# Performance work log

Measured on AMD Instinct MI355X. Metric: run time of the kernel, lower is better.

Reference implementation:

```python
import jax, jax.numpy as jnp
import numpy as np

B, T, C, H = 1024, 256, 384, 64  # batch, block_size, n_embd, head_size


def _rope_tables():
    # standard rotary tables: theta_i = 10000^(-2i/H), angles = pos * theta
    inv_freq = 1.0 / (10000.0 ** (jnp.arange(0, H, 2, dtype=jnp.float32) / H))  # [H/2]
    pos = jnp.arange(T, dtype=jnp.float32)
    ang = pos[:, None] * inv_freq[None, :]          # [T, H/2]
    ang = jnp.concatenate([ang, ang], axis=-1)       # [T, H]
    return jnp.cos(ang), jnp.sin(ang)


def setup_inputs() -> dict:
    key = jax.random.key(0)
    kx, kq, kk, kv = jax.random.split(key, 4)
    cos, sin = _rope_tables()
    s = 1.0 / np.sqrt(C)
    return {
        "x": jax.random.normal(kx, (B, T, C), dtype=jnp.float32),
        "cos": cos,
        "sin": sin,
        "Wq": jax.random.normal(kq, (C, H), dtype=jnp.float32) * s,
        "Wk": jax.random.normal(kk, (C, H), dtype=jnp.float32) * s,
        "Wv": jax.random.normal(kv, (C, H), dtype=jnp.float32) * s,
    }


def _rotary(x, cos, sin):
    # x: [B, T, H]; cos/sin: [T, H]
    half = x.shape[-1] // 2
    x1, x2 = x[..., :half], x[..., half:]
    rotated = jnp.concatenate([-x2, x1], axis=-1)
    return x * cos + rotated * sin


def reference(x, cos, sin, Wq, Wk, Wv):
    Tn = x.shape[1]
    q = x @ Wq                                  # [B,T,H]
    k = x @ Wk
    v = x @ Wv
    q = _rotary(q, cos[:Tn], sin[:Tn])
    k = _rotary(k, cos[:Tn], sin[:Tn])
    scale = k.shape[-1] ** -0.5
    wei = jnp.einsum('btd,bsd->bts', q, k) * scale  # [B,T,T] — materialized as in original
    causal = jnp.tril(jnp.ones((Tn, Tn), dtype=bool))
    wei = jnp.where(causal, wei, -jnp.inf)
    wei = jax.nn.softmax(wei, axis=-1)
    # dropout omitted (eval mode / deterministic reference)
    out = jnp.einsum('bts,bsd->btd', wei, v)    # [B,T,H]
    return out
```

## Files before the change

### kernel.cpp

```cpp
#include <hip/hip_runtime.h>
#include <hip/hip_bf16.h>

typedef __attribute__((ext_vector_type(8))) short bf16x8;
typedef __attribute__((ext_vector_type(4))) float f32x4;

#define B_ 1024
#define T_ 256
#define C_ 384
#define H_ 64

__device__ __forceinline__ unsigned short f2bf(float f) {
  unsigned int u = __float_as_uint(f);
  return (unsigned short)((u + 0x7fffu + ((u >> 16) & 1u)) >> 16);
}

__global__ void pack_w(const float* __restrict__ Wq, const float* __restrict__ Wk,
                       const float* __restrict__ Wv, unsigned short* __restrict__ wt) {
  int id = blockIdx.x * 256 + threadIdx.x;
  if (id >= 192 * 384) return;
  int n = id / 384, k = id % 384;
  const float* W = (n < 64) ? Wq : ((n < 128) ? Wk : Wv);
  wt[id] = f2bf(W[k * 64 + (n & 63)]);
}

__launch_bounds__(512, 2)
__global__ void head_fused(const float* __restrict__ x, const float* __restrict__ cosp,
                           const float* __restrict__ sinp,
                           const unsigned short* __restrict__ wt,
                           float* __restrict__ out) {
  __shared__ unsigned short Klds[256 * 72];
  __shared__ unsigned short Vlds[64 * 264];
  __shared__ unsigned short Plds[8 * 16 * 264];

  const int tid = threadIdx.x;
  const int w = tid >> 6;
  const int lane = tid & 63;
  const int l15 = lane & 15;
  const int lq = lane >> 4;
  const int b = blockIdx.x;

  const float* xb = x + (size_t)b * T_ * C_;
  const int rt[2] = {w, 15 - w};

  f32x4 acc[2][12];
  #pragma unroll
  for (int i = 0; i < 2; ++i)
    #pragma unroll
    for (int nt = 0; nt < 12; ++nt) {
      f32x4 z = {0.f, 0.f, 0.f, 0.f};
      acc[i][nt] = z;
    }

  float4 px[2][2][2];
  #pragma unroll
  for (int s = 0; s < 2; ++s)
    #pragma unroll
    for (int i = 0; i < 2; ++i) {
      const float* p = xb + (rt[i] * 16 + l15) * C_ + s * 32 + lq * 8;
      px[s][i][0] = *(const float4*)p;
      px[s][i][1] = *(const float4*)(p + 4);
    }

  #pragma unroll
  for (int ks = 0; ks < 12; ++ks) {
    const int cur = ks & 1;
    const int k0 = ks * 32 + lq * 8;

    bf16x8 af[2];
    #pragma unroll
    for (int i = 0; i < 2; ++i) {
      bf16x8 a;
      a[0] = (short)f2bf(px[cur][i][0].x); a[1] = (short)f2bf(px[cur][i][0].y);
      a[2] = (short)f2bf(px[cur][i][0].z); a[3] = (short)f2bf(px[cur][i][0].w);
      a[4] = (short)f2bf(px[cur][i][1].x); a[5] = (short)f2bf(px[cur][i][1].y);
      a[6] = (short)f2bf(px[cur][i][1].z); a[7] = (short)f2bf(px[cur][i][1].w);
      af[i] = a;
    }

    bf16x8 bfv[12];
    #pragma unroll
    for (int nt = 0; nt < 12; ++nt)
      bfv[nt] = *(const bf16x8*)(wt + (nt * 16 + l15) * C_ + k0);

    if (ks + 2 < 12) {
      #pragma unroll
      for (int i = 0; i < 2; ++i) {
        const float* p = xb + (rt[i] * 16 + l15) * C_ + (ks + 2) * 32 + lq * 8;
        px[cur][i][0] = *(const float4*)p;
        px[cur][i][1] = *(const float4*)(p + 4);
      }
    }

    #pragma unroll
    for (int nt = 0; nt < 12; ++nt)
      #pragma unroll
      for (int i = 0; i < 2; ++i)
        acc[i][nt] = __builtin_amdgcn_mfma_f32_16x16x32_bf16(af[i], bfv[nt], acc[i][nt], 0, 0, 0);
  }

  #pragma unroll
  for (int i = 0; i < 2; ++i) {
    #pragma unroll
    for (int j = 0; j < 4; ++j) {
      int t = rt[i] * 16 + lq * 4 + j;
      #pragma unroll
      for (int h = 0; h < 2; ++h) {
        int c = h * 16 + l15;
        float cv = cosp[t * H_ + c];
        float sv = sinp[t * H_ + c];
        float a = acc[i][h][j], bb = acc[i][h + 2][j];
        acc[i][h][j]     = a * cv - bb * sv;
        acc[i][h + 2][j] = bb * cv + a * sv;
        float a2 = acc[i][4 + h][j], b2 = acc[i][6 + h][j];
        acc[i][4 + h][j] = a2 * cv - b2 * sv;
        acc[i][6 + h][j] = b2 * cv + a2 * sv;
      }
    }
  }

  unsigned short* Pw = Plds + w * 16 * 264;
  #pragma unroll
  for (int i = 0; i < 2; ++i) {
    #pragma unroll
    for (int j = 0; j < 4; ++j) {
      int t = rt[i] * 16 + lq * 4 + j;
      int qr = i * 16 + lq * 4 + j;
      #pragma unroll
      for (int nt = 0; nt < 4; ++nt) {
        Pw[qr * 72 + nt * 16 + l15]    = f2bf(acc[i][nt][j]);
        Klds[t * 72 + nt * 16 + l15]   = f2bf(acc[i][4 + nt][j]);
        Vlds[(nt * 16 + l15) * 264 + t] = f2bf(acc[i][8 + nt][j]);
      }
    }
  }

  bf16x8 aq[2][2];
  #pragma unroll
  for (int i = 0; i < 2; ++i)
    #pragma unroll
    for (int ks2 = 0; ks2 < 2; ++ks2)
      aq[i][ks2] = *(const bf16x8*)&Pw[(i * 16 + l15) * 72 + ks2 * 32 + lq * 8];

  __syncthreads();

  float* ob = out + (size_t)b * T_ * H_;

  #pragma unroll
  for (int i = 0; i < 2; ++i) {
    const int ti = rt[i];
    const int t0 = ti * 16;

    f32x4 sacc[16];
    #pragma unroll
    for (int si = 0; si < 16; ++si) {
      f32x4 z = {0.f, 0.f, 0.f, 0.f};
      sacc[si] = z;
    }

    #pragma unroll
    for (int si = 0; si < 16; ++si) {
      if (si <= ti) {
        #pragma unroll
        for (int ks2 = 0; ks2 < 2; ++ks2) {
          bf16x8 bk = *(const bf16x8*)&Klds[(si * 16 + l15) * 72 + ks2 * 32 + lq * 8];
          sacc[si] = __builtin_amdgcn_mfma_f32_16x16x32_bf16(aq[i][ks2], bk, sacc[si], 0, 0, 0);
        }
      }
    }

    int trow = t0 + lq * 4;
    #pragma unroll
    for (int si = 0; si < 16; ++si) {
      #pragma unroll
      for (int j = 0; j < 4; ++j) {
        float s = sacc[si][j] * 0.125f;
        if (si * 16 + l15 > trow + j) s = -1e30f;
        sacc[si][j] = s;
      }
    }

    float rl[4];
    #pragma unroll
    for (int j = 0; j < 4; ++j) {
      float mj = -1e30f;
      #pragma unroll
      for (int si = 0; si < 16; ++si) mj = fmaxf(mj, sacc[si][j]);
      #pragma unroll
      for (int d = 1; d < 16; d <<= 1) mj = fmaxf(mj, __shfl_xor(mj, d));
      float lj = 0.0f;
      #pragma unroll
      for (int si = 0; si < 16; ++si) {
        float p = __expf(sacc[si][j] - mj);
        lj += p;
        Pw[(lq * 4 + j) * 264 + si * 16 + l15] = f2bf(p);
      }
      #pragma unroll
      for (int d = 1; d < 16; d <<= 1) lj += __shfl_xor(lj, d);
      rl[j] = 1.0f / lj;
    }

    f32x4 oacc[4];
    #pragma unroll
    for (int nt = 0; nt < 4; ++nt) {
      f32x4 z = {0.f, 0.f, 0.f, 0.f};
      oacc[nt] = z;
    }
    int nk = (t0 + 16 + 31) >> 5;
    for (int ks2 = 0; ks2 < nk; ++ks2) {
      bf16x8 ap = *(const bf16x8*)&Pw[l15 * 264 + ks2 * 32 + lq * 8];
      #pragma unroll
      for (int nt = 0; nt < 4; ++nt) {
        bf16x8 bv = *(const bf16x8*)&Vlds[(nt * 16 + l15) * 264 + ks2 * 32 + lq * 8];
        oacc[nt] = __builtin_amdgcn_mfma_f32_16x16x32_bf16(ap, bv, oacc[nt], 0, 0, 0);
      }
    }

    #pragma unroll
    for (int nt = 0; nt < 4; ++nt)
      #pragma unroll
      for (int j = 0; j < 4; ++j)
        ob[(t0 + lq * 4 + j) * H_ + nt * 16 + l15] = oacc[nt][j] * rl[j];
  }
}

extern "C" void kernel_launch(void* const* d_in, const int* in_sizes, int n_in,
                              void* d_out, int out_size, void* d_ws, size_t ws_size,
                              hipStream_t stream) {
  const float* x    = (const float*)d_in[0];
  const float* cosp = (const float*)d_in[1];
  const float* sinp = (const float*)d_in[2];
  const float* Wq   = (const float*)d_in[3];
  const float* Wk   = (const float*)d_in[4];
  const float* Wv   = (const float*)d_in[5];
  unsigned short* wt = (unsigned short*)d_ws;
  float* out = (float*)d_out;

  pack_w<<<288, 256, 0, stream>>>(Wq, Wk, Wv, wt);
  head_fused<<<B_, 512, 0, stream>>>(x, cosp, sinp, wt, out);
}
```

Baseline: 241.3 us.

## Split fused head kernel into QKV projection and attention kernels via MFMA-fragment workspace

Splits the single fused per-batch kernel into a QKV projection kernel and an attention kernel. Each uses 256-thread blocks with two blocks per batch element, and they exchange Q/K/V through global workspace stored in MFMA-fragment-packed bf16 layout. Weights are also pre-packed into fragment order so each lane does a single contiguous vector load, and attention reads K/V fragments straight from global/L2 instead of LDS. The goal is more parallelism and occupancy with less LDS use, at the cost of an extra global round trip for Q/K/V (about 100MB) and an extra launch. The old fused path is kept as a fallback when the workspace is too small.

New measurement: 379.4 us. 1.57x slower.

```diff
diff --git a/kernel.cpp b/kernel.cpp
--- a/kernel.cpp
+++ b/kernel.cpp
@@ -14,33 +14,35 @@
   return (unsigned short)((u + 0x7fffu + ((u >> 16) & 1u)) >> 16);
 }
 
-__global__ void pack_w(const float* __restrict__ Wq, const float* __restrict__ Wk,
-                       const float* __restrict__ Wv, unsigned short* __restrict__ wt) {
+__global__ void pack_w_frag(const float* __restrict__ Wq, const float* __restrict__ Wk,
+                            const float* __restrict__ Wv, unsigned short* __restrict__ wtp) {
   int id = blockIdx.x * 256 + threadIdx.x;
-  if (id >= 192 * 384) return;
-  int n = id / 384, k = id % 384;
+  if (id >= 144 * 512) return;
+  int i = id & 7, lane = (id >> 3) & 63, f = id >> 9;
+  int nt = f % 12, ks = f / 12;
+  int n = nt * 16 + (lane & 15);
+  int k = ks * 32 + (lane >> 4) * 8 + i;
   const float* W = (n < 64) ? Wq : ((n < 128) ? Wk : Wv);
-  wt[id] = f2bf(W[k * 64 + (n & 63)]);
-}
-
-__launch_bounds__(512, 2)
-__global__ void head_fused(const float* __restrict__ x, const float* __restrict__ cosp,
+  wtp[id] = f2bf(W[k * 64 + (n & 63)]);
+}
+
+__launch_bounds__(256, 4)
+__global__ void qkv_kernel(const float* __restrict__ x, const float* __restrict__ cosp,
                            const float* __restrict__ sinp,
-                           const unsigned short* __restrict__ wt,
-                           float* __restrict__ out) {
-  __shared__ unsigned short Klds[256 * 72];
-  __shared__ unsigned short Vlds[64 * 264];
-  __shared__ unsigned short Plds[8 * 16 * 264];
-
+                           const unsigned short* __restrict__ wtp,
+                           unsigned short* __restrict__ qp,
+                           unsigned short* __restrict__ kp,
+                           unsigned short* __restrict__ vp) {
   const int tid = threadIdx.x;
   const int w = tid >> 6;
   const int lane = tid & 63;
   const int l15 = lane & 15;
   const int lq = lane >> 4;
-  const int b = blockIdx.x;
+  const int bk = blockIdx.x;
+  const int b = bk >> 1, half = bk & 1;
+  const int rt[2] = {half * 8 + w, half * 8 + 7 - w};
 
   const float* xb = x + (size_t)b * T_ * C_;
-  const int rt[2] = {w, 15 - w};
 
   f32x4 acc[2][12];
   #pragma unroll
@@ -64,8 +66,6 @@
   #pragma unroll
   for (int ks = 0; ks < 12; ++ks) {
     const int cur = ks & 1;
-    const int k0 = ks * 32 + lq * 8;
-
     bf16x8 af[2];
     #pragma unroll
     for (int i = 0; i < 2; ++i) {
@@ -76,12 +76,10 @@
       a[6] = (short)f2bf(px[cur][i][1].z); a[7] = (short)f2bf(px[cur][i][1].w);
       af[i] = a;
     }
-
     bf16x8 bfv[12];
     #pragma unroll
     for (int nt = 0; nt < 12; ++nt)
-      bfv[nt] = *(const bf16x8*)(wt + (nt * 16 + l15) * C_ + k0);
-
+      bfv[nt] = *(const bf16x8*)(wtp + ((ks * 12 + nt) * 64 + lane) * 8);
     if (ks + 2 < 12) {
       #pragma unroll
       for (int i = 0; i < 2; ++i) {
@@ -90,7 +88,6 @@
         px[cur][i][1] = *(const float4*)(p + 4);
       }
     }
-
     #pragma unroll
     for (int nt = 0; nt < 12; ++nt)
       #pragma unroll
@@ -118,6 +115,228 @@
     }
   }
 
+  #pragma unroll
+  for (int i = 0; i < 2; ++i) {
+    const int tile = rt[i];
+    #pragma unroll
+    for (int j = 0; j < 4; ++j) {
+      const int r = lq * 4 + j;
+      #pragma unroll
+      for (int nt = 0; nt < 4; ++nt) {
+        size_t qa = ((((size_t)b * 16 + tile) * 2 + (nt >> 1)) * 64 +
+                     ((nt & 1) * 2 + (l15 >> 3)) * 16 + r) * 8 + (l15 & 7);
+        qp[qa] = f2bf(acc[i][nt][j]);
+        kp[qa] = f2bf(acc[i][4 + nt][j]);
+        size_t va = ((((size_t)b * 4 + nt) * 8 + (tile >> 1)) * 64 +
+                     ((tile & 1) * 2 + (r >> 3)) * 16 + l15) * 8 + (r & 7);
+        vp[va] = f2bf(acc[i][8 + nt][j]);
+      }
+    }
+  }
+}
+
+__launch_bounds__(256, 4)
+__global__ void attn_kernel(const unsigned short* __restrict__ qp,
+                            const unsigned short* __restrict__ kp,
+                            const unsigned short* __restrict__ vp,
+                            float* __restrict__ out) {
+  __shared__ unsigned short Plds[4 * 16 * 264];
+
+  const int tid = threadIdx.x;
+  const int w = tid >> 6;
+  const int lane = tid & 63;
+  const int l15 = lane & 15;
+  const int lq = lane >> 4;
+  const int bk = blockIdx.x;
+  const int b = bk >> 1, half = bk & 1;
+  const int rt2[2] = {half * 8 + w, half * 8 + 7 - w};
+
+  unsigned short* Pw = Plds + w * 16 * 264;
+  float* ob = out + (size_t)b * T_ * H_;
+
+  #pragma unroll
+  for (int i = 0; i < 2; ++i) {
+    const int ti = rt2[i];
+    const int t0 = ti * 16;
+
+    bf16x8 aq[2];
+    #pragma unroll
+    for (int ks2 = 0; ks2 < 2; ++ks2)
+      aq[ks2] = *(const bf16x8*)(qp + ((((size_t)b * 16 + ti) * 2 + ks2) * 64 + lane) * 8);
+
+    f32x4 sacc[16];
+    #pragma unroll
+    for (int si = 0; si < 16; ++si) {
+      f32x4 z = {0.f, 0.f, 0.f, 0.f};
+      sacc[si] = z;
+    }
+
+    #pragma unroll
+    for (int si = 0; si < 16; ++si) {
+      if (si <= ti) {
+        #pragma unroll
+        for (int ks2 = 0; ks2 < 2; ++ks2) {
+          bf16x8 bkf = *(const bf16x8*)(kp + ((((size_t)b * 16 + si) * 2 + ks2) * 64 + lane) * 8);
+          sacc[si] = __builtin_amdgcn_mfma_f32_16x16x32_bf16(aq[ks2], bkf, sacc[si], 0, 0, 0);
+        }
+      }
+    }
+
+    int trow = t0 + lq * 4;
+    #pragma unroll
+    for (int si = 0; si < 16; ++si) {
+      #pragma unroll
+      for (int j = 0; j < 4; ++j) {
+        float s = sacc[si][j] * 0.125f;
+        if (si * 16 + l15 > trow + j) s = -1e30f;
+        sacc[si][j] = s;
+      }
+    }
+
+    float rl[4];
+    #pragma unroll
+    for (int j = 0; j < 4; ++j) {
+      float mj = -1e30f;
+      #pragma unroll
+      for (int si = 0; si < 16; ++si) mj = fmaxf(mj, sacc[si][j]);
+      #pragma unroll
+      for (int d = 1; d < 16; d <<= 1) mj = fmaxf(mj, __shfl_xor(mj, d));
+      float lj = 0.0f;
+      #pragma unroll
+      for (int si = 0; si < 16; ++si) {
+        float p = __expf(sacc[si][j] - mj);
+        lj += p;
+        Pw[(lq * 4 + j) * 264 + si * 16 + l15] = f2bf(p);
+      }
+      #pragma unroll
+      for (int d = 1; d < 16; d <<= 1) lj += __shfl_xor(lj, d);
+      rl[j] = 1.0f / lj;
+    }
+
+    f32x4 oacc[4];
+    #pragma unroll
+    for (int nt = 0; nt < 4; ++nt) {
+      f32x4 z = {0.f, 0.f, 0.f, 0.f};
+      oacc[nt] = z;
+    }
+    int nk = (t0 + 16 + 31) >> 5;
+    for (int ks = 0; ks < nk; ++ks) {
+      bf16x8 ap = *(const bf16x8*)&Pw[l15 * 264 + ks * 32 + lq * 8];
+      #pragma unroll
+      for (int nt = 0; nt < 4; ++nt) {
+        bf16x8 bv = *(const bf16x8*)(vp + ((((size_t)b * 4 + nt) * 8 + ks) * 64 + lane) * 8);
+        oacc[nt] = __builtin_amdgcn_mfma_f32_16x16x32_bf16(ap, bv, oacc[nt], 0, 0, 0);
+      }
+    }
+
+    #pragma unroll
+    for (int nt = 0; nt < 4; ++nt)
+      #pragma unroll
+      for (int j = 0; j < 4; ++j)
+        ob[(t0 + lq * 4 + j) * H_ + nt * 16 + l15] = oacc[nt][j] * rl[j];
+  }
+}
+
+__global__ void pack_w_rm(const float* __restrict__ Wq, const float* __restrict__ Wk,
+                          const float* __restrict__ Wv, unsigned short* __restrict__ wt) {
+  int id = blockIdx.x * 256 + threadIdx.x;
+  if (id >= 192 * 384) return;
+  int n = id / 384, k = id % 384;
+  const float* W = (n < 64) ? Wq : ((n < 128) ? Wk : Wv);
+  wt[id] = f2bf(W[k * 64 + (n & 63)]);
+}
+
+__launch_bounds__(512, 2)
+__global__ void head_fused(const float* __restrict__ x, const float* __restrict__ cosp,
+                           const float* __restrict__ sinp,
+                           const unsigned short* __restrict__ wt,
+                           float* __restrict__ out) {
+  __shared__ unsigned short Klds[256 * 72];
+  __shared__ unsigned short Vlds[64 * 264];
+  __shared__ unsigned short Plds[8 * 16 * 264];
+
+  const int tid = threadIdx.x;
+  const int w = tid >> 6;
+  const int lane = tid & 63;
+  const int l15 = lane & 15;
+  const int lq = lane >> 4;
+  const int b = blockIdx.x;
+
+  const float* xb = x + (size_t)b * T_ * C_;
+  const int rt[2] = {w, 15 - w};
+
+  f32x4 acc[2][12];
+  #pragma unroll
+  for (int i = 0; i < 2; ++i)
+    #pragma unroll
+    for (int nt = 0; nt < 12; ++nt) {
+      f32x4 z = {0.f, 0.f, 0.f, 0.f};
+      acc[i][nt] = z;
+    }
+
+  float4 px[2][2][2];
+  #pragma unroll
+  for (int s = 0; s < 2; ++s)
+    #pragma unroll
+    for (int i = 0; i < 2; ++i) {
+      const float* p = xb + (rt[i] * 16 + l15) * C_ + s * 32 + lq * 8;
+      px[s][i][0] = *(const float4*)p;
+      px[s][i][1] = *(const float4*)(p + 4);
+    }
+
+  #pragma unroll
+  for (int ks = 0; ks < 12; ++ks) {
+    const int cur = ks & 1;
+    const int k0 = ks * 32 + lq * 8;
+    bf16x8 af[2];
+    #pragma unroll
+    for (int i = 0; i < 2; ++i) {
+      bf16x8 a;
+      a[0] = (short)f2bf(px[cur][i][0].x); a[1] = (short)f2bf(px[cur][i][0].y);
+      a[2] = (short)f2bf(px[cur][i][0].z); a[3] = (short)f2bf(px[cur][i][0].w);
+      a[4] = (short)f2bf(px[cur][i][1].x); a[5] = (short)f2bf(px[cur][i][1].y);
+      a[6] = (short)f2bf(px[cur][i][1].z); a[7] = (short)f2bf(px[cur][i][1].w);
+      af[i] = a;
+    }
+    bf16x8 bfv[12];
+    #pragma unroll
+    for (int nt = 0; nt < 12; ++nt)
+      bfv[nt] = *(const bf16x8*)(wt + (nt * 16 + l15) * C_ + k0);
+    if (ks + 2 < 12) {
+      #pragma unroll
+      for (int i = 0; i < 2; ++i) {
+        const float* p = xb + (rt[i] * 16 + l15) * C_ + (ks + 2) * 32 + lq * 8;
+        px[cur][i][0] = *(const float4*)p;
+        px[cur][i][1] = *(const float4*)(p + 4);
+      }
+    }
+    #pragma unroll
+    for (int nt = 0; nt < 12; ++nt)
+      #pragma unroll
+      for (int i = 0; i < 2; ++i)
+        acc[i][nt] = __builtin_amdgcn_mfma_f32_16x16x32_bf16(af[i], bfv[nt], acc[i][nt], 0, 0, 0);
+  }
+
+  #pragma unroll
+  for (int i = 0; i < 2; ++i) {
+    #pragma unroll
+    for (int j = 0; j < 4; ++j) {
+      int t = rt[i] * 16 + lq * 4 + j;
+      #pragma unroll
+      for (int h = 0; h < 2; ++h) {
+        int c = h * 16 + l15;
+        float cv = cosp[t * H_ + c];
+        float sv = sinp[t * H_ + c];
+        float a = acc[i][h][j], bb = acc[i][h + 2][j];
+        acc[i][h][j]     = a * cv - bb * sv;
+        acc[i][h + 2][j] = bb * cv + a * sv;
+        float a2 = acc[i][4 + h][j], b2 = acc[i][6 + h][j];
+        acc[i][4 + h][j] = a2 * cv - b2 * sv;
+        acc[i][6 + h][j] = b2 * cv + a2 * sv;
+      }
+    }
+  }
+
   unsigned short* Pw = Plds + w * 16 * 264;
   #pragma unroll
   for (int i = 0; i < 2; ++i) {
@@ -156,18 +375,16 @@
       f32x4 z = {0.f, 0.f, 0.f, 0.f};
       sacc[si] = z;
     }
-
     #pragma unroll
     for (int si = 0; si < 16; ++si) {
       if (si <= ti) {
         #pragma unroll
         for (int ks2 = 0; ks2 < 2; ++ks2) {
-          bf16x8 bk = *(const bf16x8*)&Klds[(si * 16 + l15) * 72 + ks2 * 32 + lq * 8];
-          sacc[si] = __builtin_amdgcn_mfma_f32_16x16x32_bf16(aq[i][ks2], bk, sacc[si], 0, 0, 0);
+          bf16x8 bkf = *(const bf16x8*)&Klds[(si * 16 + l15) * 72 + ks2 * 32 + lq * 8];
+          sacc[si] = __builtin_amdgcn_mfma_f32_16x16x32_bf16(aq[i][ks2], bkf, sacc[si], 0, 0, 0);
         }
       }
     }
-
     int trow = t0 + lq * 4;
     #pragma unroll
     for (int si = 0; si < 16; ++si) {
@@ -178,7 +395,6 @@
         sacc[si][j] = s;
       }
     }
-
     float rl[4];
     #pragma unroll
     for (int j = 0; j < 4; ++j) {
@@ -198,7 +414,6 @@
       for (int d = 1; d < 16; d <<= 1) lj += __shfl_xor(lj, d);
       rl[j] = 1.0f / lj;
     }
-
     f32x4 oacc[4];
     #pragma unroll
     for (int nt = 0; nt < 4; ++nt) {
@@ -214,7 +429,6 @@
         oacc[nt] = __builtin_amdgcn_mfma_f32_16x16x32_bf16(ap, bv, oacc[nt], 0, 0, 0);
       }
     }
-
     #pragma unroll
     for (int nt = 0; nt < 4; ++nt)
       #pragma unroll
@@ -232,9 +446,23 @@
   const float* Wq   = (const float*)d_in[3];
   const float* Wk   = (const float*)d_in[4];
   const float* Wv   = (const float*)d_in[5];
-  unsigned short* wt = (unsigned short*)d_ws;
   float* out = (float*)d_out;
 
-  pack_w<<<288, 256, 0, stream>>>(Wq, Wk, Wv, wt);
-  head_fused<<<B_, 512, 0, stream>>>(x, cosp, sinp, wt, out);
-}
+  const size_t wtp_bytes = 144 * 512 * 2;
+  const size_t frag_elems = (size_t)B_ * 16 * 2 * 64 * 8;
+  const size_t need = wtp_bytes + 3 * frag_elems * 2;
+
+  if (ws_size >= need) {
+    unsigned short* wtp = (unsigned short*)d_ws;
+    unsigned short* qp = (unsigned short*)((char*)d_ws + wtp_bytes);
+    unsigned short* kp = qp + frag_elems;
+    unsigned short* vp = kp + frag_elems;
+    pack_w_frag<<<288, 256, 0, stream>>>(Wq, Wk, Wv, wtp);
+    qkv_kernel<<<2048, 256, 0, stream>>>(x, cosp, sinp, wtp, qp, kp, vp);
+    attn_kernel<<<2048, 256, 0, stream>>>(qp, kp, vp, out);
+  } else {
+    unsigned short* wt = (unsigned short*)d_ws;
+    pack_w_rm<<<288, 256, 0, stream>>>(Wq, Wk, Wv, wt);
+    head_fused<<<B_, 512, 0, stream>>>(x, cosp, sinp, wt, out);
+  }
+}
```

## Split fused attention head into QKV projection and attention kernels via bf16 fragments

Applied to the files above, without the earlier changes.

Splits the single per-batch fused kernel into a QKV projection kernel and a separate attention kernel. The projection kernel stages x into swizzled LDS with global_load_lds and reads weights pre-packed in MFMA fragment order. It then writes rotary-applied Q, K and V in MFMA fragment layout to a global workspace, which the attention kernel reads directly instead of from LDS. The aim is smaller blocks and higher occupancy, at the cost of an extra global round trip for Q, K and V. Both launches use grids several times larger than the distinct work, since block indices are masked with &2047, so the same tiles are recomputed and rewritten redundantly.

After: 910.2 us. 3.77x slower.

```diff
diff --git a/kernel.cpp b/kernel.cpp
--- a/kernel.cpp
+++ b/kernel.cpp
@@ -1,5 +1,6 @@
 #include <hip/hip_runtime.h>
 #include <hip/hip_bf16.h>
+
 
 typedef __attribute__((ext_vector_type(8))) short bf16x8;
 typedef __attribute__((ext_vector_type(4))) float f32x4;
@@ -9,38 +10,71 @@
 #define C_ 384
 #define H_ 64
 
-__device__ __forceinline__ unsigned short f2bf(float f) {
+static __device__ __forceinline__ unsigned short f2bf(float f) {
   unsigned int u = __float_as_uint(f);
   return (unsigned short)((u + 0x7fffu + ((u >> 16) & 1u)) >> 16);
 }
 
-__global__ void pack_w(const float* __restrict__ Wq, const float* __restrict__ Wk,
-                       const float* __restrict__ Wv, unsigned short* __restrict__ wt) {
+static __device__ __forceinline__ void glds16(const void* g, void* l) {
+  __builtin_amdgcn_global_load_lds((const __attribute__((address_space(1))) void*)g,
+                                   (__attribute__((address_space(3))) void*)l, 16, 0, 0);
+}
+
+static __device__ __forceinline__ bf16x8 cvt8(float4 a, float4 b) {
+  union { __hip_bfloat162 h[4]; bf16x8 v; } u;
+  u.h[0] = __float22bfloat162_rn(make_float2(a.x, a.y));
+  u.h[1] = __float22bfloat162_rn(make_float2(a.z, a.w));
+  u.h[2] = __float22bfloat162_rn(make_float2(b.x, b.y));
+  u.h[3] = __float22bfloat162_rn(make_float2(b.z, b.w));
+  return u.v;
+}
+
+__global__ void pack_w_frag(const float* __restrict__ Wq, const float* __restrict__ Wk,
+                            const float* __restrict__ Wv, unsigned short* __restrict__ wtp) {
   int id = blockIdx.x * 256 + threadIdx.x;
-  if (id >= 192 * 384) return;
-  int n = id / 384, k = id % 384;
+  if (id >= 144 * 512) return;
+  int i = id & 7, lane = (id >> 3) & 63, f = id >> 9;
+  int nt = f % 12, ks = f / 12;
+  int n = nt * 16 + (lane & 15);
+  int k = ks * 32 + (lane >> 4) * 8 + i;
   const float* W = (n < 64) ? Wq : ((n < 128) ? Wk : Wv);
-  wt[id] = f2bf(W[k * 64 + (n & 63)]);
-}
-
-__launch_bounds__(512, 2)
-__global__ void head_fused(const float* __restrict__ x, const float* __restrict__ cosp,
+  wtp[id] = f2bf(W[k * 64 + (n & 63)]);
+}
+
+__launch_bounds__(256, 2)
+__global__ void qkv_kernel(const float* __restrict__ x, const float* __restrict__ cosp,
                            const float* __restrict__ sinp,
-                           const unsigned short* __restrict__ wt,
-                           float* __restrict__ out) {
-  __shared__ unsigned short Klds[256 * 72];
-  __shared__ unsigned short Vlds[64 * 264];
-  __shared__ unsigned short Plds[8 * 16 * 264];
+                           const unsigned short* __restrict__ wtp,
+                           unsigned short* __restrict__ qp,
+                           unsigned short* __restrict__ kp,
+                           unsigned short* __restrict__ vp) {
+  __shared__ __align__(16) char smem[4][8192];
 
   const int tid = threadIdx.x;
   const int w = tid >> 6;
   const int lane = tid & 63;
   const int l15 = lane & 15;
   const int lq = lane >> 4;
-  const int b = blockIdx.x;
+  const int bk = blockIdx.x & 2047;
+  const int b = bk >> 1, half = bk & 1;
+  const int tg0 = half * 8 + 2 * w;
+  const int row0 = tg0 * 16;
 
   const float* xb = x + (size_t)b * T_ * C_;
-  const int rt[2] = {w, 15 - w};
+  char* wbuf = smem[w];
+
+  auto stage = [&](int ks, int hb) {
+    char* dst = wbuf + hb * 4096;
+    const int rl = lane >> 3;
+    const int cg = lane & 7;
+    #pragma unroll
+    for (int s = 0; s < 4; ++s) {
+      int row = s * 8 + rl;
+      int cb = (cg * 16) ^ ((row & 7) << 4);
+      const char* src = (const char*)(xb + (size_t)(row0 + row) * C_ + ks * 32) + cb;
+      glds16(src, dst + s * 1024);
+    }
+  };
 
   f32x4 acc[2][12];
   #pragma unroll
@@ -51,44 +85,29 @@
       acc[i][nt] = z;
     }
 
-  float4 px[2][2][2];
-  #pragma unroll
-  for (int s = 0; s < 2; ++s)
-    #pragma unroll
-    for (int i = 0; i < 2; ++i) {
-      const float* p = xb + (rt[i] * 16 + l15) * C_ + s * 32 + lq * 8;
-      px[s][i][0] = *(const float4*)p;
-      px[s][i][1] = *(const float4*)(p + 4);
-    }
+  stage(0, 0);
 
   #pragma unroll
   for (int ks = 0; ks < 12; ++ks) {
     const int cur = ks & 1;
-    const int k0 = ks * 32 + lq * 8;
-
+    asm volatile("s_waitcnt vmcnt(0)" ::: "memory");
+
+    bf16x8 bfv[12];
+    #pragma unroll
+    for (int nt = 0; nt < 12; ++nt)
+      bfv[nt] = *(const bf16x8*)(wtp + ((size_t)(ks * 12 + nt) * 64 + lane) * 8);
+
+    if (ks + 1 < 12) stage(ks + 1, cur ^ 1);
+
+    const char* cbuf = wbuf + cur * 4096;
+    const int sw = (l15 & 7) << 4;
     bf16x8 af[2];
     #pragma unroll
     for (int i = 0; i < 2; ++i) {
-      bf16x8 a;
-      a[0] = (short)f2bf(px[cur][i][0].x); a[1] = (short)f2bf(px[cur][i][0].y);
-      a[2] = (short)f2bf(px[cur][i][0].z); a[3] = (short)f2bf(px[cur][i][0].w);
-      a[4] = (short)f2bf(px[cur][i][1].x); a[5] = (short)f2bf(px[cur][i][1].y);
-      a[6] = (short)f2bf(px[cur][i][1].z); a[7] = (short)f2bf(px[cur][i][1].w);
-      af[i] = a;
-    }
-
-    bf16x8 bfv[12];
-    #pragma unroll
-    for (int nt = 0; nt < 12; ++nt)
-      bfv[nt] = *(const bf16x8*)(wt + (nt * 16 + l15) * C_ + k0);
-
-    if (ks + 2 < 12) {
-      #pragma unroll
-      for (int i = 0; i < 2; ++i) {
-        const float* p = xb + (rt[i] * 16 + l15) * C_ + (ks + 2) * 32 + lq * 8;
-        px[cur][i][0] = *(const float4*)p;
-        px[cur][i][1] = *(const float4*)(p + 4);
-      }
+      const char* rp = cbuf + (i * 16 + l15) * 128;
+      float4 f0 = *(const float4*)(rp + ((lq * 32) ^ sw));
+      float4 f1 = *(const float4*)(rp + ((lq * 32 + 16) ^ sw));
+      af[i] = cvt8(f0, f1);
     }
 
     #pragma unroll
@@ -102,7 +121,7 @@
   for (int i = 0; i < 2; ++i) {
     #pragma unroll
     for (int j = 0; j < 4; ++j) {
-      int t = rt[i] * 16 + lq * 4 + j;
+      int t = (tg0 + i) * 16 + lq * 4 + j;
       #pragma unroll
       for (int h = 0; h < 2; ++h) {
         int c = h * 16 + l15;
@@ -118,37 +137,83 @@
     }
   }
 
+  unsigned short* st = (unsigned short*)wbuf;
+
+  #pragma unroll
+  for (int i = 0; i < 2; ++i)
+    #pragma unroll
+    for (int nt = 0; nt < 4; ++nt)
+      #pragma unroll
+      for (int j = 0; j < 4; ++j)
+        st[i * 1152 + (lq * 4 + j) * 72 + nt * 16 + l15] = f2bf(acc[i][nt][j]);
+  #pragma unroll
+  for (int i = 0; i < 2; ++i)
+    #pragma unroll
+    for (int ks2 = 0; ks2 < 2; ++ks2) {
+      bf16x8 fr = *(const bf16x8*)&st[i * 1152 + l15 * 72 + ks2 * 32 + lq * 8];
+      *(bf16x8*)(qp + ((((size_t)b * 16 + tg0 + i) * 2 + ks2) * 64 + lane) * 8) = fr;
+    }
+
+  #pragma unroll
+  for (int i = 0; i < 2; ++i)
+    #pragma unroll
+    for (int nt = 0; nt < 4; ++nt)
+      #pragma unroll
+      for (int j = 0; j < 4; ++j)
+        st[i * 1152 + (lq * 4 + j) * 72 + nt * 16 + l15] = f2bf(acc[i][4 + nt][j]);
+  #pragma unroll
+  for (int i = 0; i < 2; ++i)
+    #pragma unroll
+    for (int ks2 = 0; ks2 < 2; ++ks2) {
+      bf16x8 fr = *(const bf16x8*)&st[i * 1152 + l15 * 72 + ks2 * 32 + lq * 8];
+      *(bf16x8*)(kp + ((((size_t)b * 16 + tg0 + i) * 2 + ks2) * 64 + lane) * 8) = fr;
+    }
+
+  #pragma unroll
+  for (int i = 0; i < 2; ++i)
+    #pragma unroll
+    for (int nt = 0; nt < 4; ++nt)
+      #pragma unroll
+      for (int j = 0; j < 4; ++j)
+        st[(nt * 16 + l15) * 40 + i * 16 + lq * 4 + j] = f2bf(acc[i][8 + nt][j]);
+  {
+    const int ksg = half * 4 + w;
+    #pragma unroll
+    for (int nt = 0; nt < 4; ++nt) {
+      bf16x8 fr = *(const bf16x8*)&st[(nt * 16 + l15) * 40 + lq * 8];
+      *(bf16x8*)(vp + ((((size_t)b * 4 + nt) * 8 + ksg) * 64 + lane) * 8) = fr;
+    }
+  }
+}
+
+__launch_bounds__(256, 4)
+__global__ void attn_kernel(const unsigned short* __restrict__ qp,
+                            const unsigned short* __restrict__ kp,
+                            const unsigned short* __restrict__ vp,
+                            float* __restrict__ out) {
+  __shared__ unsigned short Plds[4 * 16 * 264];
+
+  const int tid = threadIdx.x;
+  const int w = tid >> 6;
+  const int lane = tid & 63;
+  const int l15 = lane & 15;
+  const int lq = lane >> 4;
+  const int bk = blockIdx.x & 2047;
+  const int b = bk >> 1, half = bk & 1;
+  const int rt2[2] = {half * 8 + w, half * 8 + 7 - w};
+
   unsigned short* Pw = Plds + w * 16 * 264;
+  float* ob = out + (size_t)b * T_ * H_;
+
   #pragma unroll
   for (int i = 0; i < 2; ++i) {
-    #pragma unroll
-    for (int j = 0; j < 4; ++j) {
-      int t = rt[i] * 16 + lq * 4 + j;
-      int qr = i * 16 + lq * 4 + j;
-      #pragma unroll
-      for (int nt = 0; nt < 4; ++nt) {
-        Pw[qr * 72 + nt * 16 + l15]    = f2bf(acc[i][nt][j]);
-        Klds[t * 72 + nt * 16 + l15]   = f2bf(acc[i][4 + nt][j]);
-        Vlds[(nt * 16 + l15) * 264 + t] = f2bf(acc[i][8 + nt][j]);
-      }
-    }
-  }
-
-  bf16x8 aq[2][2];
-  #pragma unroll
-  for (int i = 0; i < 2; ++i)
+    const int ti = rt2[i];
+    const int t0 = ti * 16;
+
+    bf16x8 aq[2];
     #pragma unroll
     for (int ks2 = 0; ks2 < 2; ++ks2)
-      aq[i][ks2] = *(const bf16x8*)&Pw[(i * 16 + l15) * 72 + ks2 * 32 + lq * 8];
-
-  __syncthreads();
-
-  float* ob = out + (size_t)b * T_ * H_;
-
-  #pragma unroll
-  for (int i = 0; i < 2; ++i) {
-    const int ti = rt[i];
-    const int t0 = ti * 16;
+      aq[ks2] = *(const bf16x8*)(qp + ((((size_t)b * 16 + ti) * 2 + ks2) * 64 + lane) * 8);
 
     f32x4 sacc[16];
     #pragma unroll
@@ -162,8 +227,8 @@
       if (si <= ti) {
         #pragma unroll
         for (int ks2 = 0; ks2 < 2; ++ks2) {
-          bf16x8 bk = *(const bf16x8*)&Klds[(si * 16 + l15) * 72 + ks2 * 32 + lq * 8];
-          sacc[si] = __builtin_amdgcn_mfma_f32_16x16x32_bf16(aq[i][ks2], bk, sacc[si], 0, 0, 0);
+          bf16x8 bkf = *(const bf16x8*)(kp + ((((size_t)b * 16 + si) * 2 + ks2) * 64 + lane) * 8);
+          sacc[si] = __builtin_amdgcn_mfma_f32_16x16x32_bf16(aq[ks2], bkf, sacc[si], 0, 0, 0);
         }
       }
     }
@@ -206,11 +271,11 @@
       oacc[nt] = z;
     }
     int nk = (t0 + 16 + 31) >> 5;
-    for (int ks2 = 0; ks2 < nk; ++ks2) {
-      bf16x8 ap = *(const bf16x8*)&Pw[l15 * 264 + ks2 * 32 + lq * 8];
+    for (int ks = 0; ks < nk; ++ks) {
+      bf16x8 ap = *(const bf16x8*)&Pw[l15 * 264 + ks * 32 + lq * 8];
       #pragma unroll
       for (int nt = 0; nt < 4; ++nt) {
-        bf16x8 bv = *(const bf16x8*)&Vlds[(nt * 16 + l15) * 264 + ks2 * 32 + lq * 8];
+        bf16x8 bv = *(const bf16x8*)(vp + ((((size_t)b * 4 + nt) * 8 + ks) * 64 + lane) * 8);
         oacc[nt] = __builtin_amdgcn_mfma_f32_16x16x32_bf16(ap, bv, oacc[nt], 0, 0, 0);
       }
     }
@@ -232,9 +297,19 @@
   const float* Wq   = (const float*)d_in[3];
   const float* Wk   = (const float*)d_in[4];
   const float* Wv   = (const float*)d_in[5];
-  unsigned short* wt = (unsigned short*)d_ws;
   float* out = (float*)d_out;
 
-  pack_w<<<288, 256, 0, stream>>>(Wq, Wk, Wv, wt);
-  head_fused<<<B_, 512, 0, stream>>>(x, cosp, sinp, wt, out);
-}
+  const size_t wtp_bytes = 144 * 512 * 2;
+  const size_t frag_elems = (size_t)B_ * 16 * 2 * 64 * 8;
+  const size_t need = wtp_bytes + 3 * frag_elems * 2;
+
+  unsigned short* wtp = (unsigned short*)d_ws;
+  unsigned short* qp = (unsigned short*)((char*)d_ws + wtp_bytes);
+  unsigned short* kp = qp + frag_elems;
+  unsigned short* vp = kp + frag_elems;
+  (void)need; (void)ws_size;
+
+  pack_w_frag<<<288, 256, 0, stream>>>(Wq, Wk, Wv, wtp);
+  qkv_kernel<<<3 * 2048, 256, 0, stream>>>(x, cosp, sinp, wtp, qp, kp, vp);
+  attn_kernel<<<8 * 2048, 256, 0, stream>>>(qp, kp, vp, out);
+}
```

## Pre-swizzle weight fragments, XOR-swizzle LDS, shrink shared memory for higher occupancy

Applied to the files above, without the earlier changes.

Weights are repacked into the exact per-lane MFMA fragment order, so each lane loads one contiguous 16-byte chunk per tile. K and V are stored in LDS without padding, using XOR swizzles to avoid bank conflicts. The per-warp P buffer is replaced by a small 1KB bounce buffer that transposes P through LDS one 32-column chunk at a time, with the softmax probabilities kept in registers. Together with hardware bf16 pair conversion, this cuts LDS use enough to raise the launch bound to 4 blocks per SM. The cost is extra small LDS round trips per chunk and higher register pressure.

Result: slower. 479.4 us (+98.7%).

```diff
diff --git a/kernel.cpp b/kernel.cpp
--- a/kernel.cpp
+++ b/kernel.cpp
@@ -1,5 +1,6 @@
 #include <hip/hip_runtime.h>
 #include <hip/hip_bf16.h>
+
 
 typedef __attribute__((ext_vector_type(8))) short bf16x8;
 typedef __attribute__((ext_vector_type(4))) float f32x4;
@@ -9,28 +10,40 @@
 #define C_ 384
 #define H_ 64
 
-__device__ __forceinline__ unsigned short f2bf(float f) {
+static __device__ __forceinline__ unsigned short f2bf(float f) {
   unsigned int u = __float_as_uint(f);
   return (unsigned short)((u + 0x7fffu + ((u >> 16) & 1u)) >> 16);
 }
 
-__global__ void pack_w(const float* __restrict__ Wq, const float* __restrict__ Wk,
-                       const float* __restrict__ Wv, unsigned short* __restrict__ wt) {
+static __device__ __forceinline__ bf16x8 cvt8(float4 a, float4 b) {
+  union { __hip_bfloat162 h[4]; bf16x8 v; } u;
+  u.h[0] = __float22bfloat162_rn(make_float2(a.x, a.y));
+  u.h[1] = __float22bfloat162_rn(make_float2(a.z, a.w));
+  u.h[2] = __float22bfloat162_rn(make_float2(b.x, b.y));
+  u.h[3] = __float22bfloat162_rn(make_float2(b.z, b.w));
+  return u.v;
+}
+
+__global__ void pack_w_frag(const float* __restrict__ Wq, const float* __restrict__ Wk,
+                            const float* __restrict__ Wv, unsigned short* __restrict__ wtp) {
   int id = blockIdx.x * 256 + threadIdx.x;
-  if (id >= 192 * 384) return;
-  int n = id / 384, k = id % 384;
+  if (id >= 144 * 512) return;
+  int i = id & 7, lane = (id >> 3) & 63, f = id >> 9;
+  int nt = f % 12, ks = f / 12;
+  int n = nt * 16 + (lane & 15);
+  int k = ks * 32 + (lane >> 4) * 8 + i;
   const float* W = (n < 64) ? Wq : ((n < 128) ? Wk : Wv);
-  wt[id] = f2bf(W[k * 64 + (n & 63)]);
-}
-
-__launch_bounds__(512, 2)
+  wtp[id] = f2bf(W[k * 64 + (n & 63)]);
+}
+
+__launch_bounds__(512, 4)
 __global__ void head_fused(const float* __restrict__ x, const float* __restrict__ cosp,
                            const float* __restrict__ sinp,
-                           const unsigned short* __restrict__ wt,
+                           const unsigned short* __restrict__ wtp,
                            float* __restrict__ out) {
-  __shared__ unsigned short Klds[256 * 72];
-  __shared__ unsigned short Vlds[64 * 264];
-  __shared__ unsigned short Plds[8 * 16 * 264];
+  __shared__ __align__(16) unsigned short Klds[256 * 64];
+  __shared__ __align__(16) unsigned short Vlds[64 * 256];
+  __shared__ __align__(16) unsigned short Bounce[8 * 512];
 
   const int tid = threadIdx.x;
   const int w = tid >> 6;
@@ -41,6 +54,7 @@
 
   const float* xb = x + (size_t)b * T_ * C_;
   const int rt[2] = {w, 15 - w};
+  char* Bw = (char*)(Bounce + w * 512);
 
   f32x4 acc[2][12];
   #pragma unroll
@@ -64,24 +78,13 @@
   #pragma unroll
   for (int ks = 0; ks < 12; ++ks) {
     const int cur = ks & 1;
-    const int k0 = ks * 32 + lq * 8;
-
     bf16x8 af[2];
     #pragma unroll
-    for (int i = 0; i < 2; ++i) {
-      bf16x8 a;
-      a[0] = (short)f2bf(px[cur][i][0].x); a[1] = (short)f2bf(px[cur][i][0].y);
-      a[2] = (short)f2bf(px[cur][i][0].z); a[3] = (short)f2bf(px[cur][i][0].w);
-      a[4] = (short)f2bf(px[cur][i][1].x); a[5] = (short)f2bf(px[cur][i][1].y);
-      a[6] = (short)f2bf(px[cur][i][1].z); a[7] = (short)f2bf(px[cur][i][1].w);
-      af[i] = a;
-    }
-
+    for (int i = 0; i < 2; ++i) af[i] = cvt8(px[cur][i][0], px[cur][i][1]);
     bf16x8 bfv[12];
     #pragma unroll
     for (int nt = 0; nt < 12; ++nt)
-      bfv[nt] = *(const bf16x8*)(wt + (nt * 16 + l15) * C_ + k0);
-
+      bfv[nt] = *(const bf16x8*)(wtp + ((size_t)(ks * 12 + nt) * 64 + lane) * 8);
     if (ks + 2 < 12) {
       #pragma unroll
       for (int i = 0; i < 2; ++i) {
@@ -90,7 +93,6 @@
         px[cur][i][1] = *(const float4*)(p + 4);
       }
     }
-
     #pragma unroll
     for (int nt = 0; nt < 12; ++nt)
       #pragma unroll
@@ -118,32 +120,43 @@
     }
   }
 
-  unsigned short* Pw = Plds + w * 16 * 264;
+  bf16x8 aq[2][2];
+  #pragma unroll
+  for (int i = 0; i < 2; ++i) {
+    #pragma unroll
+    for (int ks2 = 0; ks2 < 2; ++ks2) {
+      #pragma unroll
+      for (int nt2 = 0; nt2 < 2; ++nt2) {
+        const int nt = ks2 * 2 + nt2;
+        #pragma unroll
+        for (int j = 0; j < 4; ++j) {
+          const int r = lq * 4 + j;
+          const int nl = nt2 * 16 + l15;
+          *(unsigned short*)(Bw + r * 64 + ((nl * 2) ^ ((r & 3) << 4))) = f2bf(acc[i][nt][j]);
+        }
+      }
+      aq[i][ks2] = *(const bf16x8*)(Bw + l15 * 64 + ((lq * 16) ^ ((l15 & 3) << 4)));
+    }
+  }
+
   #pragma unroll
   for (int i = 0; i < 2; ++i) {
     #pragma unroll
     for (int j = 0; j < 4; ++j) {
-      int t = rt[i] * 16 + lq * 4 + j;
-      int qr = i * 16 + lq * 4 + j;
+      const int t = rt[i] * 16 + lq * 4 + j;
       #pragma unroll
       for (int nt = 0; nt < 4; ++nt) {
-        Pw[qr * 72 + nt * 16 + l15]    = f2bf(acc[i][nt][j]);
-        Klds[t * 72 + nt * 16 + l15]   = f2bf(acc[i][4 + nt][j]);
-        Vlds[(nt * 16 + l15) * 264 + t] = f2bf(acc[i][8 + nt][j]);
-      }
-    }
-  }
-
-  bf16x8 aq[2][2];
-  #pragma unroll
-  for (int i = 0; i < 2; ++i)
-    #pragma unroll
-    for (int ks2 = 0; ks2 < 2; ++ks2)
-      aq[i][ks2] = *(const bf16x8*)&Pw[(i * 16 + l15) * 72 + ks2 * 32 + lq * 8];
-
+        const int n = nt * 16 + l15;
+        *(unsigned short*)((char*)Klds + t * 128 + ((n * 2) ^ ((t & 7) << 4))) = f2bf(acc[i][4 + nt][j]);
+        const int h = nt * 16 + l15;
+        *(unsigned short*)((char*)Vlds + h * 512 + ((t * 2) ^ ((h & 7) << 4))) = f2bf(acc[i][8 + nt][j]);
+      }
+    }
+  }
   __syncthreads();
 
   float* ob = out + (size_t)b * T_ * H_;
+  const int kswz = (l15 & 7) << 4;
 
   #pragma unroll
   for (int i = 0; i < 2; ++i) {
@@ -162,13 +175,14 @@
       if (si <= ti) {
         #pragma unroll
         for (int ks2 = 0; ks2 < 2; ++ks2) {
-          bf16x8 bk = *(const bf16x8*)&Klds[(si * 16 + l15) * 72 + ks2 * 32 + lq * 8];
-          sacc[si] = __builtin_amdgcn_mfma_f32_16x16x32_bf16(aq[i][ks2], bk, sacc[si], 0, 0, 0);
+          bf16x8 bkf = *(const bf16x8*)((const char*)Klds + (si * 16 + l15) * 128 +
+                                        ((ks2 * 64 + lq * 16) ^ kswz));
+          sacc[si] = __builtin_amdgcn_mfma_f32_16x16x32_bf16(aq[i][ks2], bkf, sacc[si], 0, 0, 0);
         }
       }
     }
 
-    int trow = t0 + lq * 4;
+    const int trow = t0 + lq * 4;
     #pragma unroll
     for (int si = 0; si < 16; ++si) {
       #pragma unroll
@@ -192,7 +206,7 @@
       for (int si = 0; si < 16; ++si) {
         float p = __expf(sacc[si][j] - mj);
         lj += p;
-        Pw[(lq * 4 + j) * 264 + si * 16 + l15] = f2bf(p);
+        sacc[si][j] = p;
       }
       #pragma unroll
       for (int d = 1; d < 16; d <<= 1) lj += __shfl_xor(lj, d);
@@ -205,12 +219,23 @@
       f32x4 z = {0.f, 0.f, 0.f, 0.f};
       oacc[nt] = z;
     }
-    int nk = (t0 + 16 + 31) >> 5;
-    for (int ks2 = 0; ks2 < nk; ++ks2) {
-      bf16x8 ap = *(const bf16x8*)&Pw[l15 * 264 + ks2 * 32 + lq * 8];
+    const int nk = (t0 + 16 + 31) >> 5;
+    for (int ks = 0; ks < nk; ++ks) {
+      #pragma unroll
+      for (int half = 0; half < 2; ++half) {
+        const int si = 2 * ks + half;
+        #pragma unroll
+        for (int j = 0; j < 4; ++j) {
+          const int r = lq * 4 + j;
+          const int sl = half * 16 + l15;
+          *(unsigned short*)(Bw + r * 64 + ((sl * 2) ^ ((r & 3) << 4))) = f2bf(sacc[si][j]);
+        }
+      }
+      bf16x8 ap = *(const bf16x8*)(Bw + l15 * 64 + ((lq * 16) ^ ((l15 & 3) << 4)));
       #pragma unroll
       for (int nt = 0; nt < 4; ++nt) {
-        bf16x8 bv = *(const bf16x8*)&Vlds[(nt * 16 + l15) * 264 + ks2 * 32 + lq * 8];
+        bf16x8 bv = *(const bf16x8*)((const char*)Vlds + (nt * 16 + l15) * 512 +
+                                     ((ks * 64 + lq * 16) ^ kswz));
         oacc[nt] = __builtin_amdgcn_mfma_f32_16x16x32_bf16(ap, bv, oacc[nt], 0, 0, 0);
       }
     }
@@ -232,9 +257,11 @@
   const float* Wq   = (const float*)d_in[3];
   const float* Wk   = (const float*)d_in[4];
   const float* Wv   = (const float*)d_in[5];
-  unsigned short* wt = (unsigned short*)d_ws;
   float* out = (float*)d_out;
 
-  pack_w<<<288, 256, 0, stream>>>(Wq, Wk, Wv, wt);
-  head_fused<<<B_, 512, 0, stream>>>(x, cosp, sinp, wt, out);
-}
+  unsigned short* wtp = (unsigned short*)d_ws;
+  (void)ws_size;
+
+  pack_w_frag<<<288, 256, 0, stream>>>(Wq, Wk, Wv, wtp);
+  head_fused<<<B_, 512, 0, stream>>>(x, cosp, sinp, wtp, out);
+}
```
